# Kernel tuning notes

Measured on AMD Instinct MI355X. Metric: run time of the kernel, lower is better.

## Reference

```python
import jax, jax.numpy as jnp
import numpy as np

B, S, D = 2, 2048, 1024
H, HD = 16, 64

def setup_inputs() -> dict:
    key = jax.random.key(0)
    k1, k2, k3 = jax.random.split(key, 3)
    x = jax.random.normal(k1, (B, S, D), dtype=jnp.float32)
    w_qkv = jax.random.normal(k2, (3 * D, D), dtype=jnp.float32) * (D ** -0.5)
    w_out = jax.random.normal(k3, (D, D), dtype=jnp.float32) * (D ** -0.5)
    return {"x": x, "w_qkv": w_qkv, "w_out": w_out}

def reference(x, w_qkv, w_out):
    scale = HD ** -0.5
    # qkv projection: torch Linear applies x @ W.T
    qkv = jnp.einsum('bsd,ed->bse', x, w_qkv)            # [B,S,3D]
    qkv = qkv.reshape(B, S, 3, H, HD)
    q, k, v = qkv[:, :, 0], qkv[:, :, 1], qkv[:, :, 2]   # [B,S,H,HD]
    # scores: explicit matmul-softmax-matmul (unfused, as in source)
    scores = jnp.einsum('bqhd,bkhd->bhqk', q, k) * scale  # [B,H,S,S]
    attn = jax.nn.softmax(scores, axis=-1)
    out = jnp.einsum('bhqk,bkhd->bqhd', attn, v)          # [B,S,H,HD]
    out = out.reshape(B, S, D)
    return jnp.einsum('bsd,ed->bse', out, w_out)
```

## Files before the change

kernel.cpp:

```cpp
#include <hip/hip_runtime.h>
#include <hip/hip_bf16.h>
#include <math.h>

#define B_ 2
#define S_ 2048
#define D_ 1024
#define H_ 16
#define HD_ 64

typedef short bf16x8 __attribute__((ext_vector_type(8)));
typedef short bf16x4 __attribute__((ext_vector_type(4)));
typedef float f32x4 __attribute__((ext_vector_type(4)));

#define MFMA32(a, b, c) __builtin_amdgcn_mfma_f32_16x16x32_bf16(a, b, c, 0, 0, 0)
#define MFMA16(a, b, c) __builtin_amdgcn_mfma_f32_16x16x16bf16_1k(a, b, c, 0, 0, 0)

static __device__ __forceinline__ unsigned short f2bf(float f) {
    union { float f; unsigned u; } v = {f};
    return (unsigned short)((v.u + 0x7fffu + ((v.u >> 16) & 1u)) >> 16);
}

static __device__ __forceinline__ unsigned pk2bf(float a, float b) {
    __hip_bfloat162 h = __float22bfloat162_rn(make_float2(a, b));
    unsigned r;
    __builtin_memcpy(&r, &h, 4);
    return r;
}

static __device__ __forceinline__ void gl2lds16(const void* g, void* l) {
    __builtin_amdgcn_global_load_lds((const __attribute__((address_space(1))) unsigned int*)g,
                                     (__attribute__((address_space(3))) unsigned int*)l,
                                     16, 0, 0);
}

__global__ __launch_bounds__(256) void cvt_all(const float* __restrict__ x,
                                               const float* __restrict__ wq,
                                               const float* __restrict__ wo,
                                               unsigned short* __restrict__ xb,
                                               unsigned short* __restrict__ wqb,
                                               unsigned short* __restrict__ wob) {
    const int N0 = 1048576, N1 = 786432, N2 = 262144;
    int stride = gridDim.x * blockDim.x;
    for (int i = blockIdx.x * blockDim.x + threadIdx.x; i < N0 + N1 + N2; i += stride) {
        const float4* src; ushort4* dst; int j;
        if (i < N0)            { src = (const float4*)x;  dst = (ushort4*)xb;  j = i; }
        else if (i < N0 + N1)  { src = (const float4*)wq; dst = (ushort4*)wqb; j = i - N0; }
        else                   { src = (const float4*)wo; dst = (ushort4*)wob; j = i - N0 - N1; }
        float4 v = src[j];
        ushort4 o;
        o.x = f2bf(v.x); o.y = f2bf(v.y); o.z = f2bf(v.z); o.w = f2bf(v.w);
        dst[j] = o;
    }
}

template <int BN>
__global__ __launch_bounds__(256) void gemm_nt_b(const unsigned short* __restrict__ A,
                                                 const unsigned short* __restrict__ Bm,
                                                 void* __restrict__ Cout,
                                                 int M, int N, int K, int c_bf16) {
    constexpr int BM = 128, BK = 32;
    constexpr int MI = (BN == 128) ? 4 : 2;
    constexpr int NI = 4;
    constexpr int SEGS = (BM + BN) / 16;
    __shared__ unsigned short As[BM * BK];
    __shared__ unsigned short Bs[BN * BK];

    const int tid = threadIdx.x;
    const int wave = tid >> 6, lane = tid & 63;
    const int m16 = lane & 15, quad = lane >> 4;
    const int wrow = (BN == 128) ? (wave >> 1) * 64 : wave * 32;
    const int wcol = (BN == 128) ? (wave & 1) * 64 : 0;
    const int row0 = blockIdx.y * BM, col0 = blockIdx.x * BN;

    const int lrow = lane >> 2;
    const int lk = (lane & 3) * 8;

    f32x4 acc[MI][NI] = {};

    for (int k0 = 0; k0 < K; k0 += BK) {
        __syncthreads();
        for (int s = wave; s < SEGS; s += 4) {
            if (s < BM / 16) {
                gl2lds16(&A[(size_t)(row0 + s * 16 + lrow) * K + k0 + lk],
                         &As[s * 16 * BK]);
            } else {
                int t = s - BM / 16;
                gl2lds16(&Bm[(size_t)(col0 + t * 16 + lrow) * K + k0 + lk],
                         &Bs[t * 16 * BK]);
            }
        }
        __asm__ volatile("s_waitcnt vmcnt(0)" ::: "memory");
        __syncthreads();

        bf16x8 af[MI], bfr[NI];
        #pragma unroll
        for (int mi = 0; mi < MI; ++mi)
            af[mi] = *(const bf16x8*)&As[(wrow + mi * 16 + m16) * BK + quad * 8];
        #pragma unroll
        for (int ni = 0; ni < NI; ++ni)
            bfr[ni] = *(const bf16x8*)&Bs[(wcol + ni * 16 + m16) * BK + quad * 8];
        #pragma unroll
        for (int mi = 0; mi < MI; ++mi)
            #pragma unroll
            for (int ni = 0; ni < NI; ++ni)
                acc[mi][ni] = MFMA32(af[mi], bfr[ni], acc[mi][ni]);
    }

    #pragma unroll
    for (int mi = 0; mi < MI; ++mi) {
        #pragma unroll
        for (int r = 0; r < 4; ++r) {
            size_t grow = row0 + wrow + mi * 16 + quad * 4 + r;
            #pragma unroll
            for (int ni = 0; ni < NI; ++ni) {
                size_t gcol = col0 + wcol + ni * 16 + m16;
                if (c_bf16)
                    ((unsigned short*)Cout)[grow * N + gcol] = f2bf(acc[mi][ni][r]);
                else
                    ((float*)Cout)[grow * N + gcol] = acc[mi][ni][r];
            }
        }
    }
}

__global__ __launch_bounds__(256) void attn_mfma(const unsigned short* __restrict__ qkv,
                                                 unsigned short* __restrict__ out) {
    constexpr int LDKS = 72;
    constexpr int LDV = 68;
    __shared__ unsigned short Ks[2][64 * LDKS];
    __shared__ unsigned short Vt[2][64 * LDV];

    const int id = blockIdx.x;
    const int bh = ((id >> 3) & 3) * 8 + (id & 7);
    const int b = bh >> 4, h = bh & 15;
    const int q0 = (id >> 5) * 128;

    const int tid = threadIdx.x;
    const int wave = tid >> 6, lane = tid & 63;
    const int m16 = lane & 15, quad = lane >> 4;

    const float C1 = 0.125f * 1.44269504089f;
    const float C2 = 10.0f * 1.44269504089f;

    bf16x8 qf0[2], qf1[2];
    #pragma unroll
    for (int g = 0; g < 2; ++g) {
        const unsigned short* qrow =
            qkv + ((size_t)b * S_ + q0 + wave * 32 + g * 16 + m16) * (3 * D_) + h * HD_;
        qf0[g] = *(const bf16x8*)(qrow + quad * 8);
        qf1[g] = *(const bf16x8*)(qrow + 32 + quad * 8);
    }

    f32x4 o[2][4] = {};
    f32x4 ol[2] = {};
    const bf16x4 onesf = {(short)0x3F80, (short)0x3F80, (short)0x3F80, (short)0x3F80};

    const unsigned short* kbase = qkv + (size_t)b * S_ * 3 * D_ + D_ + h * HD_;
    const unsigned short* vbase = qkv + (size_t)b * S_ * 3 * D_ + 2 * D_ + h * HD_;

    const int kr = tid >> 3;
    const int kc8 = (tid & 7) * 8;
    const int vrp = (tid >> 4) * 2;
    const int vc4 = (tid & 15) * 4;
    const int vxr = 4 * ((tid & 15) & 7);

    int vaddr[4][4];
    #pragma unroll
    for (int dt = 0; dt < 4; ++dt) {
        int d = dt * 16 + m16;
        int xr = 4 * ((d >> 2) & 7);
        #pragma unroll
        for (int nt = 0; nt < 4; ++nt)
            vaddr[dt][nt] = d * LDV + ((nt * 16 + quad * 4) ^ xr);
    }

    uint4 kg[2];
    ushort4 vg[2][2];

    auto loadTile = [&](int t) {
        const size_t kt = (size_t)t * 64;
        #pragma unroll
        for (int i = 0; i < 2; ++i) {
            kg[i] = *(const uint4*)(kbase + (kt + kr + i * 32) * (3 * D_) + kc8);
            const unsigned short* vp = vbase + (kt + vrp + i * 32) * (3 * D_) + vc4;
            vg[i][0] = *(const ushort4*)vp;
            vg[i][1] = *(const ushort4*)(vp + 3 * D_);
        }
    };
    auto storeTile = [&](int bufi) {
        #pragma unroll
        for (int i = 0; i < 2; ++i) {
            *(uint4*)&Ks[bufi][(kr + i * 32) * LDKS + kc8] = kg[i];
            int koff = (vrp + i * 32) ^ vxr;
            unsigned short* vb_ = &Vt[bufi][0];
            *(unsigned*)&vb_[(vc4 + 0) * LDV + koff] = (unsigned)vg[i][0].x | ((unsigned)vg[i][1].x << 16);
            *(unsigned*)&vb_[(vc4 + 1) * LDV + koff] = (unsigned)vg[i][0].y | ((unsigned)vg[i][1].y << 16);
            *(unsigned*)&vb_[(vc4 + 2) * LDV + koff] = (unsigned)vg[i][0].z | ((unsigned)vg[i][1].z << 16);
            *(unsigned*)&vb_[(vc4 + 3) * LDV + koff] = (unsigned)vg[i][0].w | ((unsigned)vg[i][1].w << 16);
        }
    };

    loadTile(0);
    storeTile(0);
    __syncthreads();

    for (int t = 0; t < S_ / 64; ++t) {
        const int buf = t & 1;
        const bool more = (t + 1) < (S_ / 64);

        if (more) loadTile(t + 1);

        bf16x4 pf[2][4];
        #pragma unroll
        for (int nt = 0; nt < 4; ++nt) {
            const unsigned short* kp = &Ks[buf][(nt * 16 + m16) * LDKS];
            bf16x8 kf0 = *(const bf16x8*)(kp + quad * 8);
            bf16x8 kf1 = *(const bf16x8*)(kp + 32 + quad * 8);
            #pragma unroll
            for (int g = 0; g < 2; ++g) {
                f32x4 z = {0.f, 0.f, 0.f, 0.f};
                z = MFMA32(kf0, qf0[g], z);
                z = MFMA32(kf1, qf1[g], z);
                float p0 = __builtin_amdgcn_exp2f(z[0] * C1 - C2);
                float p1 = __builtin_amdgcn_exp2f(z[1] * C1 - C2);
                float p2 = __builtin_amdgcn_exp2f(z[2] * C1 - C2);
                float p3 = __builtin_amdgcn_exp2f(z[3] * C1 - C2);
                union { unsigned u[2]; bf16x4 v; } pk;
                pk.u[0] = pk2bf(p0, p1);
                pk.u[1] = pk2bf(p2, p3);
                pf[g][nt] = pk.v;
                ol[g] = MFMA16(pf[g][nt], onesf, ol[g]);
            }
        }

        #pragma unroll
        for (int nt = 0; nt < 4; ++nt)
            #pragma unroll
            for (int dt = 0; dt < 4; ++dt) {
                bf16x4 vf = *(const bf16x4*)&Vt[buf][vaddr[dt][nt]];
                o[0][dt] = MFMA16(pf[0][nt], vf, o[0][dt]);
                o[1][dt] = MFMA16(pf[1][nt], vf, o[1][dt]);
            }

        if (more) storeTile(buf ^ 1);
        __syncthreads();
    }

    #pragma unroll
    for (int g = 0; g < 2; ++g)
        #pragma unroll
        for (int r = 0; r < 4; ++r) {
            float inv = 1.f / ol[g][r];
            size_t row = (size_t)b * S_ + q0 + wave * 32 + g * 16 + quad * 4 + r;
            unsigned short* op = out + row * D_ + h * HD_;
            #pragma unroll
            for (int dt = 0; dt < 4; ++dt)
                op[dt * 16 + m16] = f2bf(o[g][dt][r] * inv);
        }
}

extern "C" void kernel_launch(void* const* d_in, const int* in_sizes, int n_in,
                              void* d_out, int out_size, void* d_ws, size_t ws_size,
                              hipStream_t stream) {
    const float* x     = (const float*)d_in[0];
    const float* w_qkv = (const float*)d_in[1];
    const float* w_out = (const float*)d_in[2];
    float* out = (float*)d_out;

    const size_t n_x = (size_t)B_ * S_ * D_;
    const size_t n_wqkv = (size_t)3 * D_ * D_;
    const size_t n_wout = (size_t)D_ * D_;

    unsigned short* xb    = (unsigned short*)d_ws;
    unsigned short* wqkvb = xb + n_x;
    unsigned short* woutb = wqkvb + n_wqkv;
    unsigned short* qkvb  = woutb + n_wout;
    unsigned short* attnb = qkvb + (size_t)B_ * S_ * 3 * D_;

    dim3 blk(256);

    cvt_all<<<2048, blk, 0, stream>>>(x, w_qkv, w_out, xb, wqkvb, woutb);

    gemm_nt_b<128><<<dim3(3 * D_ / 128, B_ * S_ / 128), blk, 0, stream>>>(
        xb, wqkvb, qkvb, B_ * S_, 3 * D_, D_, 1);

    attn_mfma<<<512, blk, 0, stream>>>(qkvb, attnb);

    gemm_nt_b<64><<<dim3(D_ / 64, B_ * S_ / 128), blk, 0, stream>>>(
        attnb, woutb, out, B_ * S_, D_, D_, 0);
}
```

Before: 214.0 us.

## Pre-transpose V and stream K/V tiles into LDS via direct global-to-LDS loads

Adds a separate kernel that writes V in [bh, d, s] order, so the attention kernel can fetch both K and V tiles with direct global-to-LDS loads (gl2lds16) into XOR-swizzled, unpadded shared buffers. The old register-staged loads and the scattered transposing LDS stores for V go away, and prefetch becomes two tiles ahead with waitcnt plus a barrier. The cost is an extra launch plus a round trip of V through memory and extra workspace. The kernel relies on a gl2lds16 helper that is assumed to exist in the hidden part of the file.

```diff
diff --git a/kernel.cpp b/kernel.cpp
--- a/kernel.cpp
+++ b/kernel.cpp
@@ -123,12 +123,38 @@
     }
 }
 
+__global__ __launch_bounds__(256) void transpose_v(const unsigned short* __restrict__ qkv,
+                                                   unsigned short* __restrict__ vt) {
+    __shared__ unsigned short T[64 * 72];
+    const int bid = blockIdx.x;
+    const int bh = bid & 31, st = bid >> 5;
+    const int b = bh >> 4, h = bh & 15;
+    const int tid = threadIdx.x;
+
+    #pragma unroll
+    for (int i = 0; i < 2; ++i) {
+        int idx = tid + i * 256;
+        int r = idx >> 3, c8 = (idx & 7) * 8;
+        *(uint4*)&T[r * 72 + c8] =
+            *(const uint4*)(qkv + (size_t)(b * S_ + st * 64 + r) * (3 * D_) + 2 * D_ + h * HD_ + c8);
+    }
+    __syncthreads();
+    #pragma unroll
+    for (int i = 0; i < 2; ++i) {
+        int idx = tid + i * 256;
+        int d = idx >> 3, s8 = (idx & 7) * 8;
+        unsigned short a[8];
+        #pragma unroll
+        for (int j = 0; j < 8; ++j) a[j] = T[(s8 + j) * 72 + d];
+        *(uint4*)(vt + ((size_t)bh * 64 + d) * S_ + st * 64 + s8) = *(uint4*)a;
+    }
+}
+
 __global__ __launch_bounds__(256) void attn_mfma(const unsigned short* __restrict__ qkv,
+                                                 const unsigned short* __restrict__ vt,
                                                  unsigned short* __restrict__ out) {
-    constexpr int LDKS = 72;
-    constexpr int LDV = 68;
-    __shared__ unsigned short Ks[2][64 * LDKS];
-    __shared__ unsigned short Vt[2][64 * LDV];
+    __shared__ unsigned short Ks[2][64 * 64];
+    __shared__ unsigned short Vs[2][64 * 64];
 
     const int id = blockIdx.x;
     const int bh = ((id >> 3) & 3) * 8 + (id & 7);
@@ -156,66 +182,49 @@
     const bf16x4 onesf = {(short)0x3F80, (short)0x3F80, (short)0x3F80, (short)0x3F80};
 
     const unsigned short* kbase = qkv + (size_t)b * S_ * 3 * D_ + D_ + h * HD_;
-    const unsigned short* vbase = qkv + (size_t)b * S_ * 3 * D_ + 2 * D_ + h * HD_;
-
-    const int kr = tid >> 3;
-    const int kc8 = (tid & 7) * 8;
-    const int vrp = (tid >> 4) * 2;
-    const int vc4 = (tid & 15) * 4;
-    const int vxr = 4 * ((tid & 15) & 7);
+    const unsigned short* vtbase = vt + (size_t)bh * 64 * S_;
+
+    const int lr8 = lane >> 3;
+    const int lsrc = (lane & 7) ^ lr8;
 
     int vaddr[4][4];
     #pragma unroll
     for (int dt = 0; dt < 4; ++dt) {
         int d = dt * 16 + m16;
-        int xr = 4 * ((d >> 2) & 7);
-        #pragma unroll
-        for (int nt = 0; nt < 4; ++nt)
-            vaddr[dt][nt] = d * LDV + ((nt * 16 + quad * 4) ^ xr);
-    }
-
-    uint4 kg[2];
-    ushort4 vg[2][2];
-
-    auto loadTile = [&](int t) {
-        const size_t kt = (size_t)t * 64;
+        #pragma unroll
+        for (int nt = 0; nt < 4; ++nt) {
+            int kc = nt * 2 + (quad >> 1);
+            vaddr[dt][nt] = d * 64 + ((kc ^ (m16 & 7)) * 8) + (quad & 1) * 4;
+        }
+    }
+
+    auto issueDMA = [&](int t, int buf) {
         #pragma unroll
         for (int i = 0; i < 2; ++i) {
-            kg[i] = *(const uint4*)(kbase + (kt + kr + i * 32) * (3 * D_) + kc8);
-            const unsigned short* vp = vbase + (kt + vrp + i * 32) * (3 * D_) + vc4;
-            vg[i][0] = *(const ushort4*)vp;
-            vg[i][1] = *(const ushort4*)(vp + 3 * D_);
+            int gi = wave * 2 + i;
+            int r = gi * 8 + lr8;
+            gl2lds16(kbase + (size_t)(t * 64 + r) * (3 * D_) + lsrc * 8,
+                     &Ks[buf][gi * 512]);
+            gl2lds16(vtbase + (size_t)r * S_ + t * 64 + lsrc * 8,
+                     &Vs[buf][gi * 512]);
         }
     };
-    auto storeTile = [&](int bufi) {
-        #pragma unroll
-        for (int i = 0; i < 2; ++i) {
-            *(uint4*)&Ks[bufi][(kr + i * 32) * LDKS + kc8] = kg[i];
-            int koff = (vrp + i * 32) ^ vxr;
-            unsigned short* vb_ = &Vt[bufi][0];
-            *(unsigned*)&vb_[(vc4 + 0) * LDV + koff] = (unsigned)vg[i][0].x | ((unsigned)vg[i][1].x << 16);
-            *(unsigned*)&vb_[(vc4 + 1) * LDV + koff] = (unsigned)vg[i][0].y | ((unsigned)vg[i][1].y << 16);
-            *(unsigned*)&vb_[(vc4 + 2) * LDV + koff] = (unsigned)vg[i][0].z | ((unsigned)vg[i][1].z << 16);
-            *(unsigned*)&vb_[(vc4 + 3) * LDV + koff] = (unsigned)vg[i][0].w | ((unsigned)vg[i][1].w << 16);
-        }
-    };
-
-    loadTile(0);
-    storeTile(0);
+
+    issueDMA(0, 0);
+    __asm__ volatile("s_waitcnt vmcnt(0)" ::: "memory");
     __syncthreads();
+    issueDMA(1, 1);
 
     for (int t = 0; t < S_ / 64; ++t) {
         const int buf = t & 1;
-        const bool more = (t + 1) < (S_ / 64);
-
-        if (more) loadTile(t + 1);
 
         bf16x4 pf[2][4];
         #pragma unroll
         for (int nt = 0; nt < 4; ++nt) {
-            const unsigned short* kp = &Ks[buf][(nt * 16 + m16) * LDKS];
-            bf16x8 kf0 = *(const bf16x8*)(kp + quad * 8);
-            bf16x8 kf1 = *(const bf16x8*)(kp + 32 + quad * 8);
+            int row = nt * 16 + m16;
+            int a0 = row * 64 + ((quad ^ (m16 & 7)) * 8);
+            bf16x8 kf0 = *(const bf16x8*)&Ks[buf][a0];
+            bf16x8 kf1 = *(const bf16x8*)&Ks[buf][a0 ^ 32];
             #pragma unroll
             for (int g = 0; g < 2; ++g) {
                 f32x4 z = {0.f, 0.f, 0.f, 0.f};
@@ -237,13 +246,14 @@
         for (int nt = 0; nt < 4; ++nt)
             #pragma unroll
             for (int dt = 0; dt < 4; ++dt) {
-                bf16x4 vf = *(const bf16x4*)&Vt[buf][vaddr[dt][nt]];
+                bf16x4 vf = *(const bf16x4*)&Vs[buf][vaddr[dt][nt]];
                 o[0][dt] = MFMA16(pf[0][nt], vf, o[0][dt]);
                 o[1][dt] = MFMA16(pf[1][nt], vf, o[1][dt]);
             }
 
-        if (more) storeTile(buf ^ 1);
+        __asm__ volatile("s_waitcnt vmcnt(0)" ::: "memory");
         __syncthreads();
+        if (t + 2 < S_ / 64) issueDMA(t + 2, buf);
     }
 
     #pragma unroll
@@ -276,6 +286,7 @@
     unsigned short* woutb = wqkvb + n_wqkv;
     unsigned short* qkvb  = woutb + n_wout;
     unsigned short* attnb = qkvb + (size_t)B_ * S_ * 3 * D_;
+    unsigned short* vtb   = attnb + n_x;
 
     dim3 blk(256);
 
@@ -284,7 +295,9 @@
     gemm_nt_b<128><<<dim3(3 * D_ / 128, B_ * S_ / 128), blk, 0, stream>>>(
         xb, wqkvb, qkvb, B_ * S_, 3 * D_, D_, 1);
 
-    attn_mfma<<<512, blk, 0, stream>>>(qkvb, attnb);
+    transpose_v<<<1024, blk, 0, stream>>>(qkvb, vtb);
+
+    attn_mfma<<<512, blk, 0, stream>>>(qkvb, vtb, attnb);
 
     gemm_nt_b<64><<<dim3(D_ / 64, B_ * S_ / 128), blk, 0, stream>>>(
         attnb, woutb, out, B_ * S_, D_, D_, 0);
```

New measurement: 208.7 us. 1.03x faster.
